# Kernel tuning notes

Hardware: AMD Instinct MI355X
Metric: run time of the kernel (lower is better)

## Reference

```python
import jax, jax.numpy as jnp
import numpy as np
import math

E = 512      # embed_dim
H = 8        # num_heads
D = E // H   # head_embed_dim
B = 1
S = 4096

def setup_inputs() -> dict:
    key = jax.random.key(0)
    ks = jax.random.split(key, 9)
    s = 1.0 / math.sqrt(E)
    return {
        "Q": jax.random.normal(ks[0], (B, S, E), dtype=jnp.float32),
        "K": jax.random.normal(ks[1], (B, S, E), dtype=jnp.float32),
        "V": jax.random.normal(ks[2], (B, S, E), dtype=jnp.float32),
        "W_qk": jax.random.uniform(ks[3], (E, E), jnp.float32, -s, s),
        "b_qk": jax.random.uniform(ks[4], (E,), jnp.float32, -s, s),
        "W_v": jax.random.uniform(ks[5], (E, E), jnp.float32, -s, s),
        "b_v": jax.random.uniform(ks[6], (E,), jnp.float32, -s, s),
        "W_out": jax.random.uniform(ks[7], (E, E), jnp.float32, -s, s),
        "b_out": jax.random.uniform(ks[8], (E,), jnp.float32, -s, s),
    }

def reference(Q, K, V, W_qk, b_qk, W_v, b_v, W_out, b_out):
    # shared qk projection (torch Linear: x @ W.T + b)
    q = Q @ W_qk.T + b_qk
    k = K @ W_qk.T + b_qk
    v = V @ W_v.T + b_v
    # NOTE: original uses .view(B, H, S, D) -- a pure reshape, no transpose
    q = q.reshape(B, H, S, D)
    k = k.reshape(B, H, S, D)
    v = v.reshape(B, H, S, D)
    scores = jnp.einsum("bhsd,bhtd->bhst", q, k) / math.sqrt(D)
    attn = jax.nn.softmax(scores, axis=-1)
    out = jnp.einsum("bhst,bhtd->bhsd", attn, v)
    out = out.reshape(B, S, E)  # matches .view merge
    return out @ W_out.T + b_out
```

## Files before the change

kernel.cpp:

```cpp
#include <hip/hip_runtime.h>
#include <hip/hip_bf16.h>
#include <math.h>

typedef __hip_bfloat16 hbf16;
typedef __attribute__((ext_vector_type(4))) float f32x4;
typedef __attribute__((ext_vector_type(8))) __bf16 bf16x8;

#define MFMA16(a, b, c) __builtin_amdgcn_mfma_f32_16x16x32_bf16((a), (b), (c), 0, 0, 0)

__device__ __forceinline__ void gload_lds16(const hbf16* g, hbf16* l) {
  __builtin_amdgcn_global_load_lds(
      (const __attribute__((address_space(1))) void*)g,
      (__attribute__((address_space(3))) void*)l, 16, 0, 0);
}

__device__ __forceinline__ void cvt4(const float* __restrict__ s, hbf16* __restrict__ d, int i) {
  float4 v = reinterpret_cast<const float4*>(s)[i];
  union { hbf16 h[4]; uint2 u; } pk;
  pk.h[0] = __float2bfloat16(v.x);
  pk.h[1] = __float2bfloat16(v.y);
  pk.h[2] = __float2bfloat16(v.z);
  pk.h[3] = __float2bfloat16(v.w);
  reinterpret_cast<uint2*>(d)[i] = pk.u;
}

__global__ __launch_bounds__(256) void cvt3_kernel(
    const float* __restrict__ s0, const float* __restrict__ s1, const float* __restrict__ s2,
    hbf16* __restrict__ d0, hbf16* __restrict__ d1, hbf16* __restrict__ d2, int n4) {
  int stride = gridDim.x * blockDim.x;
  for (int i = blockIdx.x * blockDim.x + threadIdx.x; i < n4; i += stride) {
    cvt4(s0, d0, i);
    cvt4(s1, d1, i);
    cvt4(s2, d2, i);
  }
}

__device__ __forceinline__ void gemm_core_128(
    const hbf16* __restrict__ A, const hbf16* __restrict__ B, int K, int bm, int bn,
    hbf16* Alds, hbf16* Blds, f32x4 (&acc)[4][4]) {
  const int tid = threadIdx.x;
  const int lane = tid & 63;
  const int wave = tid >> 6;
  const int wr = wave >> 1, wc = wave & 1;
  const int l15 = lane & 15, lg = lane >> 4;
  const hbf16* Abase = A + (size_t)bm * 128 * K;
  const hbf16* Bbase = B + (size_t)bn * 128 * K;
  for (int k0 = 0; k0 < K; k0 += 32) {
    if (k0) __syncthreads();
#pragma unroll
    for (int rr = 0; rr < 2; ++rr) {
      int chunk = rr * 256 + tid;
      int row = chunk >> 2;
      int c8 = (chunk & 3) << 3;
      gload_lds16(Abase + (size_t)row * K + k0 + c8, Alds + (rr * 4 + wave) * 512);
      gload_lds16(Bbase + (size_t)row * K + k0 + c8, Blds + (rr * 4 + wave) * 512);
    }
    __syncthreads();
    bf16x8 af[4], bfv[4];
#pragma unroll
    for (int m = 0; m < 4; ++m)
      af[m] = *reinterpret_cast<const bf16x8*>(&Alds[(wr * 64 + m * 16 + l15) * 32 + lg * 8]);
#pragma unroll
    for (int n = 0; n < 4; ++n)
      bfv[n] = *reinterpret_cast<const bf16x8*>(&Blds[(wc * 64 + n * 16 + l15) * 32 + lg * 8]);
#pragma unroll
    for (int m = 0; m < 4; ++m)
#pragma unroll
      for (int n = 0; n < 4; ++n)
        acc[m][n] = MFMA16(af[m], bfv[n], acc[m][n]);
  }
}

__global__ __launch_bounds__(256) void proj_qk_kernel(
    const hbf16* __restrict__ Qb, const hbf16* __restrict__ Kb,
    const hbf16* __restrict__ Wqk, const float* __restrict__ bqk,
    hbf16* __restrict__ qp, hbf16* __restrict__ kp) {
  __shared__ __align__(16) hbf16 Alds[128 * 32];
  __shared__ __align__(16) hbf16 Blds[128 * 32];
  const int z = blockIdx.y;
  const hbf16* A = z ? Kb : Qb;
  hbf16* outp = z ? kp : qp;
  const int bm = blockIdx.x & 31, bn = blockIdx.x >> 5;

  f32x4 acc[4][4];
  const f32x4 zero = {0.f, 0.f, 0.f, 0.f};
#pragma unroll
  for (int m = 0; m < 4; ++m)
#pragma unroll
    for (int n = 0; n < 4; ++n) acc[m][n] = zero;

  gemm_core_128(A, Wqk, 512, bm, bn, Alds, Blds, acc);

  const float qscale = z ? 1.0f : 0.125f * 1.4426950408889634f;

  const int lane = threadIdx.x & 63, wave = threadIdx.x >> 6;
  const int wr = wave >> 1, wc = wave & 1;
  const int l15 = lane & 15, lg = lane >> 4;
  const int row0 = bm * 128 + wr * 64;
  const int col0 = bn * 128 + wc * 64;
#pragma unroll
  for (int m = 0; m < 4; ++m) {
#pragma unroll
    for (int n = 0; n < 4; ++n) {
      const int col = col0 + n * 16 + l15;
      const float bsv = bqk[col];
#pragma unroll
      for (int j = 0; j < 4; ++j) {
        const int row = row0 + m * 16 + lg * 4 + j;
        outp[(size_t)row * 512 + col] = __float2bfloat16((acc[m][n][j] + bsv) * qscale);
      }
    }
  }
}

__global__ __launch_bounds__(256) void proj_v_kernel(
    const hbf16* __restrict__ Wv, const hbf16* __restrict__ Vb,
    const float* __restrict__ bv, hbf16* __restrict__ vT) {
  __shared__ __align__(16) hbf16 Alds[128 * 32];
  __shared__ __align__(16) hbf16 Blds[128 * 32];
  const int bm = blockIdx.x >> 5;
  const int bn = blockIdx.x & 31;

  f32x4 acc[4][4];
  const f32x4 zero = {0.f, 0.f, 0.f, 0.f};
#pragma unroll
  for (int m = 0; m < 4; ++m)
#pragma unroll
    for (int n = 0; n < 4; ++n) acc[m][n] = zero;

  gemm_core_128(Wv, Vb, 512, bm, bn, Alds, Blds, acc);

  const int lane = threadIdx.x & 63, wave = threadIdx.x >> 6;
  const int wr = wave >> 1, wc = wave & 1;
  const int l15 = lane & 15, lg = lane >> 4;
  const int row0 = bm * 128 + wr * 64;
  const int col0 = bn * 128 + wc * 64;
#pragma unroll
  for (int m = 0; m < 4; ++m) {
#pragma unroll
    for (int n = 0; n < 4; ++n) {
      const int col = col0 + n * 16 + l15;
#pragma unroll
      for (int j = 0; j < 4; ++j) {
        const int row = row0 + m * 16 + lg * 4 + j;
        const int h = col >> 9;
        const int p = ((col & 511) << 3) + (row >> 6);
        const int d = row & 63;
        vT[(size_t)h * 262144 + (size_t)d * 4096 + p] =
            __float2bfloat16(acc[m][n][j] + bv[row]);
      }
    }
  }
}

__global__ __launch_bounds__(256) void out_gemm_kernel(
    const hbf16* __restrict__ A, const hbf16* __restrict__ B, const float* __restrict__ bias,
    float* __restrict__ out) {
  __shared__ __align__(16) hbf16 Alds[128 * 32];
  __shared__ __align__(16) hbf16 Blds[128 * 32];
  const int bm = blockIdx.x & 31, bn = blockIdx.x >> 5;
  f32x4 acc[4][4];
  const f32x4 zero = {0.f, 0.f, 0.f, 0.f};
#pragma unroll
  for (int m = 0; m < 4; ++m)
#pragma unroll
    for (int n = 0; n < 4; ++n) acc[m][n] = zero;

  gemm_core_128(A, B, 512, bm, bn, Alds, Blds, acc);

  const int lane = threadIdx.x & 63, wave = threadIdx.x >> 6;
  const int wr = wave >> 1, wc = wave & 1;
  const int l15 = lane & 15, lg = lane >> 4;
  const int row0 = bm * 128 + wr * 64;
  const int col0 = bn * 128 + wc * 64;
#pragma unroll
  for (int m = 0; m < 4; ++m) {
#pragma unroll
    for (int n = 0; n < 4; ++n) {
      const int col = col0 + n * 16 + l15;
      const float bsv = bias[col];
#pragma unroll
      for (int j = 0; j < 4; ++j) {
        const int row = row0 + m * 16 + lg * 4 + j;
        out[(size_t)row * 512 + col] = acc[m][n][j] + bsv;
      }
    }
  }
}

__device__ __forceinline__ void stage64(const hbf16* __restrict__ g, int gstride,
                                        hbf16* tile, int wave, int lane) {
#pragma unroll
  for (int ii = 0; ii < 2; ++ii) {
    const int i = wave * 2 + ii;
    const int row = i * 8 + (lane >> 3);
    const int ce = ((lane & 7) ^ (lane >> 3)) << 3;
    gload_lds16(g + (size_t)row * gstride + ce, tile + i * 512);
  }
}

template <bool DIRECT>
__global__ __launch_bounds__(256) void attn_kernel2(
    const hbf16* __restrict__ qp, const hbf16* __restrict__ kp,
    const hbf16* __restrict__ vT, hbf16* __restrict__ ao,
    float* __restrict__ Opart, float* __restrict__ Lpart,
    int kv_per_split, int nwg) {
  const int lin = blockIdx.x + 32 * (blockIdx.y + 8 * blockIdx.z);
  const int chunk = nwg >> 3;
  const int swz = (lin & 7) * chunk + (lin >> 3);
  const int qt = swz & 31;
  const int h = (swz >> 5) & 7;
  const int split = swz >> 8;

  const hbf16* qh = qp + (size_t)h * 262144;
  const hbf16* kh = kp + (size_t)h * 262144;
  const hbf16* vh = vT + (size_t)h * 262144;

  const int lane = threadIdx.x & 63, wave = threadIdx.x >> 6;
  const int l15 = lane & 15, lg = lane >> 4;
  const int qrow0 = qt * 128 + wave * 32;
  const int kv0 = split * kv_per_split;
  const int nkt = kv_per_split >> 6;

  __shared__ __align__(16) hbf16 Kt[2][4096];
  __shared__ __align__(16) hbf16 Vt[2][4096];
  __shared__ __align__(16) hbf16 Pl[4][2][16][68];

  bf16x8 qf[2][2];
#pragma unroll
  for (int rb = 0; rb < 2; ++rb)
#pragma unroll
    for (int dc = 0; dc < 2; ++dc)
      qf[rb][dc] = *reinterpret_cast<const bf16x8*>(
          &qh[(size_t)(qrow0 + rb * 16 + l15) * 64 + dc * 32 + lg * 8]);

  float lsum[2][4];
  f32x4 oacc[2][4];
  const f32x4 zero = {0.f, 0.f, 0.f, 0.f};
#pragma unroll
  for (int rb = 0; rb < 2; ++rb)
#pragma unroll
    for (int j = 0; j < 4; ++j) lsum[rb][j] = 0.f;
#pragma unroll
  for (int rb = 0; rb < 2; ++rb)
#pragma unroll
    for (int db = 0; db < 4; ++db) oacc[rb][db] = zero;

  stage64(kh + (size_t)kv0 * 64, 64, Kt[0], wave, lane);
  stage64(vh + kv0, 4096, Vt[0], wave, lane);
  __syncthreads();

  int cur = 0;
  for (int t = 0; t < nkt; ++t) {
    if (t + 1 < nkt) {
      const int kb = kv0 + (t + 1) * 64;
      stage64(kh + (size_t)kb * 64, 64, Kt[cur ^ 1], wave, lane);
      stage64(vh + kb, 4096, Vt[cur ^ 1], wave, lane);
    }
    const hbf16* Kc = Kt[cur];
    const hbf16* Vc = Vt[cur];

    f32x4 s[2][4];
#pragma unroll
    for (int rb = 0; rb < 2; ++rb)
#pragma unroll
      for (int cb = 0; cb < 4; ++cb) s[rb][cb] = zero;
#pragma unroll
    for (int cb = 0; cb < 4; ++cb) {
      const int krow = cb * 16 + l15;
      const int sw = l15 & 7;
#pragma unroll
      for (int dc = 0; dc < 2; ++dc) {
        bf16x8 kf = *reinterpret_cast<const bf16x8*>(
            &Kc[krow * 64 + (((dc * 4 + lg) ^ sw) << 3)]);
#pragma unroll
        for (int rb = 0; rb < 2; ++rb) s[rb][cb] = MFMA16(qf[rb][dc], kf, s[rb][cb]);
      }
    }

#pragma unroll
    for (int rb = 0; rb < 2; ++rb)
#pragma unroll
      for (int cb = 0; cb < 4; ++cb)
#pragma unroll
        for (int j = 0; j < 4; ++j) {
          const float p = exp2f(s[rb][cb][j]);
          lsum[rb][j] += p;
          Pl[wave][rb][lg * 4 + j][cb * 16 + l15] = __float2bfloat16(p);
        }
    bf16x8 pa[2][2];
#pragma unroll
    for (int rb = 0; rb < 2; ++rb)
#pragma unroll
      for (int kc = 0; kc < 2; ++kc)
        pa[rb][kc] = *reinterpret_cast<const bf16x8*>(&Pl[wave][rb][l15][kc * 32 + lg * 8]);

#pragma unroll
    for (int db = 0; db < 4; ++db) {
      const int vrow = db * 16 + l15;
      const int sw = l15 & 7;
#pragma unroll
      for (int kc = 0; kc < 2; ++kc) {
        bf16x8 vf = *reinterpret_cast<const bf16x8*>(
            &Vc[vrow * 64 + (((kc * 4 + lg) ^ sw) << 3)]);
#pragma unroll
        for (int rb = 0; rb < 2; ++rb) oacc[rb][db] = MFMA16(pa[rb][kc], vf, oacc[rb][db]);
      }
    }
    __syncthreads();
    cur ^= 1;
  }

#pragma unroll
  for (int rb = 0; rb < 2; ++rb)
#pragma unroll
    for (int j = 0; j < 4; ++j) {
#pragma unroll
      for (int d = 1; d < 16; d <<= 1) lsum[rb][j] += __shfl_xor(lsum[rb][j], d);
    }
  if (DIRECT) {
    hbf16* oh = ao + (size_t)h * 262144;
#pragma unroll
    for (int rb = 0; rb < 2; ++rb)
#pragma unroll
      for (int j = 0; j < 4; ++j) {
        const float inv = 1.f / lsum[rb][j];
        const int row = qrow0 + rb * 16 + lg * 4 + j;
#pragma unroll
        for (int db = 0; db < 4; ++db)
          oh[(size_t)row * 64 + db * 16 + l15] = __float2bfloat16(oacc[rb][db][j] * inv);
      }
  } else {
    const size_t hrow0 = (size_t)split * 32768 + (size_t)h * 4096;
#pragma unroll
    for (int rb = 0; rb < 2; ++rb)
#pragma unroll
      for (int j = 0; j < 4; ++j) {
        const int row = qrow0 + rb * 16 + lg * 4 + j;
#pragma unroll
        for (int db = 0; db < 4; ++db)
          Opart[(hrow0 + row) * 64 + db * 16 + l15] = oacc[rb][db][j];
        if (l15 == 0) Lpart[hrow0 + row] = lsum[rb][j];
      }
  }
}

__global__ __launch_bounds__(256) void attn_combine_kernel(
    const float* __restrict__ Opart, const float* __restrict__ Lpart,
    hbf16* __restrict__ ao, int splits) {
  const int t = threadIdx.x;
  const int hrow = blockIdx.x * 64 + (t >> 2);
  const int d0 = (t & 3) * 16;
  float denom = 0.f;
  for (int s = 0; s < splits; ++s) denom += Lpart[s * 32768 + hrow];
  const float inv = 1.f / denom;
  float4 acc[4] = {};
  for (int s = 0; s < splits; ++s) {
    const float4* p = reinterpret_cast<const float4*>(
        Opart + ((size_t)s * 32768 + hrow) * 64 + d0);
#pragma unroll
    for (int i = 0; i < 4; ++i) {
      float4 v = p[i];
      acc[i].x += v.x; acc[i].y += v.y; acc[i].z += v.z; acc[i].w += v.w;
    }
  }
  union { hbf16 h[16]; uint4 u[2]; } pk;
#pragma unroll
  for (int i = 0; i < 4; ++i) {
    pk.h[i * 4 + 0] = __float2bfloat16(acc[i].x * inv);
    pk.h[i * 4 + 1] = __float2bfloat16(acc[i].y * inv);
    pk.h[i * 4 + 2] = __float2bfloat16(acc[i].z * inv);
    pk.h[i * 4 + 3] = __float2bfloat16(acc[i].w * inv);
  }
  uint4* dst = reinterpret_cast<uint4*>(ao + (size_t)hrow * 64 + d0);
  dst[0] = pk.u[0];
  dst[1] = pk.u[1];
}

extern "C" void kernel_launch(void* const* d_in, const int* in_sizes, int n_in,
                              void* d_out, int out_size, void* d_ws, size_t ws_size,
                              hipStream_t stream) {
  const float* Q = (const float*)d_in[0];
  const float* K = (const float*)d_in[1];
  const float* V = (const float*)d_in[2];
  const float* Wqk = (const float*)d_in[3];
  const float* bqk = (const float*)d_in[4];
  const float* Wv = (const float*)d_in[5];
  const float* bv = (const float*)d_in[6];
  const float* Wout = (const float*)d_in[7];
  const float* bout = (const float*)d_in[8];
  float* out = (float*)d_out;

  const size_t NE = (size_t)4096 * 512;
  const size_t WE = (size_t)512 * 512;
  hbf16* ws = (hbf16*)d_ws;
  hbf16* Qb = ws;
  hbf16* Kb = Qb + NE;
  hbf16* Vb = Kb + NE;
  hbf16* Wqkb = Vb + NE;
  hbf16* Wvb = Wqkb + WE;
  hbf16* Woutb = Wvb + WE;
  hbf16* qp = Woutb + WE;
  hbf16* kp = qp + NE;
  hbf16* vT = kp + NE;
  hbf16* ao = vT + NE;

  const size_t base_bytes = (((size_t)(7 * NE + 3 * WE) * 2) + 255) & ~(size_t)255;
  const size_t per_split_bytes = ((size_t)32768 * 64 + 32768) * 4;
  int splits = 1;
  if (ws_size >= base_bytes + 4 * per_split_bytes) splits = 4;
  else if (ws_size >= base_bytes + 2 * per_split_bytes) splits = 2;
  float* Opart = (float*)((char*)d_ws + base_bytes);
  float* Lpart = Opart + (size_t)splits * 32768 * 64;

  cvt3_kernel<<<2048, 256, 0, stream>>>(Q, K, V, Qb, Kb, Vb, (int)(NE / 4));
  cvt3_kernel<<<256, 256, 0, stream>>>(Wqk, Wv, Wout, Wqkb, Wvb, Woutb, (int)(WE / 4));
  proj_qk_kernel<<<dim3(128, 2), 256, 0, stream>>>(Qb, Kb, Wqkb, bqk, qp, kp);
  proj_v_kernel<<<128, 256, 0, stream>>>(Wvb, Vb, bv, vT);
  if (splits == 1) {
    attn_kernel2<true><<<dim3(32, 8, 1), 256, 0, stream>>>(
        qp, kp, vT, ao, nullptr, nullptr, 4096, 256);
  } else {
    attn_kernel2<false><<<dim3(32, 8, splits), 256, 0, stream>>>(
        qp, kp, vT, nullptr, Opart, Lpart, 4096 / splits, 256 * splits);
    attn_combine_kernel<<<512, 256, 0, stream>>>(Opart, Lpart, ao, splits);
  }
  out_gemm_kernel<<<128, 256, 0, stream>>>(ao, Woutb, bout, out);
}
```

Baseline: 209.9 us.

## Fuse conversion and projection launches; keep P in registers via transposed scores

The two fp32-to-bf16 conversion launches are merged into one kernel, and the QK and V projection kernels are merged into a single three-slice grid, which removes launch overhead and lets the projections run concurrently. In the attention kernel the score MFMA operands are swapped so S comes out transposed. P is then repacked into bf16 A-fragments with cross-lane shuffles instead of a round trip through LDS, which drops the per-wave P buffer and its barrier traffic. The row sums now reduce over lane groups, launch bounds request 4 blocks per CU, and the extra shuffles add VALU work.

```diff
diff --git a/kernel.cpp b/kernel.cpp
--- a/kernel.cpp
+++ b/kernel.cpp
@@ -24,14 +24,22 @@
   reinterpret_cast<uint2*>(d)[i] = pk.u;
 }
 
-__global__ __launch_bounds__(256) void cvt3_kernel(
-    const float* __restrict__ s0, const float* __restrict__ s1, const float* __restrict__ s2,
-    hbf16* __restrict__ d0, hbf16* __restrict__ d1, hbf16* __restrict__ d2, int n4) {
+__global__ __launch_bounds__(256) void cvt_all_kernel(
+    const float* __restrict__ Q, const float* __restrict__ K, const float* __restrict__ V,
+    const float* __restrict__ Wqk, const float* __restrict__ Wv, const float* __restrict__ Wout,
+    hbf16* __restrict__ Qb, hbf16* __restrict__ Kb, hbf16* __restrict__ Vb,
+    hbf16* __restrict__ Wqkb, hbf16* __restrict__ Wvb, hbf16* __restrict__ Woutb,
+    int n4big, int n4w) {
   int stride = gridDim.x * blockDim.x;
-  for (int i = blockIdx.x * blockDim.x + threadIdx.x; i < n4; i += stride) {
-    cvt4(s0, d0, i);
-    cvt4(s1, d1, i);
-    cvt4(s2, d2, i);
+  for (int i = blockIdx.x * blockDim.x + threadIdx.x; i < n4big; i += stride) {
+    cvt4(Q, Qb, i);
+    cvt4(K, Kb, i);
+    cvt4(V, Vb, i);
+    if (i < n4w) {
+      cvt4(Wqk, Wqkb, i);
+      cvt4(Wv, Wvb, i);
+      cvt4(Wout, Woutb, i);
+    }
   }
 }
 
@@ -71,55 +79,17 @@
   }
 }
 
-__global__ __launch_bounds__(256) void proj_qk_kernel(
-    const hbf16* __restrict__ Qb, const hbf16* __restrict__ Kb,
-    const hbf16* __restrict__ Wqk, const float* __restrict__ bqk,
-    hbf16* __restrict__ qp, hbf16* __restrict__ kp) {
+__global__ __launch_bounds__(256) void proj_fused_kernel(
+    const hbf16* __restrict__ Qb, const hbf16* __restrict__ Kb, const hbf16* __restrict__ Vb,
+    const hbf16* __restrict__ Wqk, const hbf16* __restrict__ Wv,
+    const float* __restrict__ bqk, const float* __restrict__ bv,
+    hbf16* __restrict__ qp, hbf16* __restrict__ kp, hbf16* __restrict__ vT) {
   __shared__ __align__(16) hbf16 Alds[128 * 32];
   __shared__ __align__(16) hbf16 Blds[128 * 32];
   const int z = blockIdx.y;
-  const hbf16* A = z ? Kb : Qb;
-  hbf16* outp = z ? kp : qp;
-  const int bm = blockIdx.x & 31, bn = blockIdx.x >> 5;
-
-  f32x4 acc[4][4];
-  const f32x4 zero = {0.f, 0.f, 0.f, 0.f};
-#pragma unroll
-  for (int m = 0; m < 4; ++m)
-#pragma unroll
-    for (int n = 0; n < 4; ++n) acc[m][n] = zero;
-
-  gemm_core_128(A, Wqk, 512, bm, bn, Alds, Blds, acc);
-
-  const float qscale = z ? 1.0f : 0.125f * 1.4426950408889634f;
-
   const int lane = threadIdx.x & 63, wave = threadIdx.x >> 6;
   const int wr = wave >> 1, wc = wave & 1;
   const int l15 = lane & 15, lg = lane >> 4;
-  const int row0 = bm * 128 + wr * 64;
-  const int col0 = bn * 128 + wc * 64;
-#pragma unroll
-  for (int m = 0; m < 4; ++m) {
-#pragma unroll
-    for (int n = 0; n < 4; ++n) {
-      const int col = col0 + n * 16 + l15;
-      const float bsv = bqk[col];
-#pragma unroll
-      for (int j = 0; j < 4; ++j) {
-        const int row = row0 + m * 16 + lg * 4 + j;
-        outp[(size_t)row * 512 + col] = __float2bfloat16((acc[m][n][j] + bsv) * qscale);
-      }
-    }
-  }
-}
-
-__global__ __launch_bounds__(256) void proj_v_kernel(
-    const hbf16* __restrict__ Wv, const hbf16* __restrict__ Vb,
-    const float* __restrict__ bv, hbf16* __restrict__ vT) {
-  __shared__ __align__(16) hbf16 Alds[128 * 32];
-  __shared__ __align__(16) hbf16 Blds[128 * 32];
-  const int bm = blockIdx.x >> 5;
-  const int bn = blockIdx.x & 31;
 
   f32x4 acc[4][4];
   const f32x4 zero = {0.f, 0.f, 0.f, 0.f};
@@ -128,26 +98,47 @@
 #pragma unroll
     for (int n = 0; n < 4; ++n) acc[m][n] = zero;
 
-  gemm_core_128(Wv, Vb, 512, bm, bn, Alds, Blds, acc);
-
-  const int lane = threadIdx.x & 63, wave = threadIdx.x >> 6;
-  const int wr = wave >> 1, wc = wave & 1;
-  const int l15 = lane & 15, lg = lane >> 4;
-  const int row0 = bm * 128 + wr * 64;
-  const int col0 = bn * 128 + wc * 64;
-#pragma unroll
-  for (int m = 0; m < 4; ++m) {
-#pragma unroll
-    for (int n = 0; n < 4; ++n) {
-      const int col = col0 + n * 16 + l15;
-#pragma unroll
-      for (int j = 0; j < 4; ++j) {
-        const int row = row0 + m * 16 + lg * 4 + j;
-        const int h = col >> 9;
-        const int p = ((col & 511) << 3) + (row >> 6);
-        const int d = row & 63;
-        vT[(size_t)h * 262144 + (size_t)d * 4096 + p] =
-            __float2bfloat16(acc[m][n][j] + bv[row]);
+  if (z < 2) {
+    const hbf16* A = z ? Kb : Qb;
+    hbf16* outp = z ? kp : qp;
+    const int bm = blockIdx.x & 31, bn = blockIdx.x >> 5;
+    gemm_core_128(A, Wqk, 512, bm, bn, Alds, Blds, acc);
+    const float qscale = z ? 1.0f : 0.125f * 1.4426950408889634f;
+    const int row0 = bm * 128 + wr * 64;
+    const int col0 = bn * 128 + wc * 64;
+#pragma unroll
+    for (int m = 0; m < 4; ++m) {
+#pragma unroll
+      for (int n = 0; n < 4; ++n) {
+        const int col = col0 + n * 16 + l15;
+        const float bsv = bqk[col];
+#pragma unroll
+        for (int j = 0; j < 4; ++j) {
+          const int row = row0 + m * 16 + lg * 4 + j;
+          outp[(size_t)row * 512 + col] = __float2bfloat16((acc[m][n][j] + bsv) * qscale);
+        }
+      }
+    }
+  } else {
+    const int bm = blockIdx.x >> 5;
+    const int bn = blockIdx.x & 31;
+    gemm_core_128(Wv, Vb, 512, bm, bn, Alds, Blds, acc);
+    const int row0 = bm * 128 + wr * 64;
+    const int col0 = bn * 128 + wc * 64;
+#pragma unroll
+    for (int m = 0; m < 4; ++m) {
+#pragma unroll
+      for (int n = 0; n < 4; ++n) {
+        const int col = col0 + n * 16 + l15;
+#pragma unroll
+        for (int j = 0; j < 4; ++j) {
+          const int row = row0 + m * 16 + lg * 4 + j;
+          const int h = col >> 9;
+          const int p = ((col & 511) << 3) + (row >> 6);
+          const int d = row & 63;
+          vT[(size_t)h * 262144 + (size_t)d * 4096 + p] =
+              __float2bfloat16(acc[m][n][j] + bv[row]);
+        }
       }
     }
   }
@@ -200,7 +191,7 @@
 }
 
 template <bool DIRECT>
-__global__ __launch_bounds__(256) void attn_kernel2(
+__global__ __launch_bounds__(256, 4) void attn_kernel3(
     const hbf16* __restrict__ qp, const hbf16* __restrict__ kp,
     const hbf16* __restrict__ vT, hbf16* __restrict__ ao,
     float* __restrict__ Opart, float* __restrict__ Lpart,
@@ -224,7 +215,6 @@
 
   __shared__ __align__(16) hbf16 Kt[2][4096];
   __shared__ __align__(16) hbf16 Vt[2][4096];
-  __shared__ __align__(16) hbf16 Pl[4][2][16][68];
 
   bf16x8 qf[2][2];
 #pragma unroll
@@ -234,13 +224,9 @@
       qf[rb][dc] = *reinterpret_cast<const bf16x8*>(
           &qh[(size_t)(qrow0 + rb * 16 + l15) * 64 + dc * 32 + lg * 8]);
 
-  float lsum[2][4];
+  float lsum[2] = {0.f, 0.f};
   f32x4 oacc[2][4];
   const f32x4 zero = {0.f, 0.f, 0.f, 0.f};
-#pragma unroll
-  for (int rb = 0; rb < 2; ++rb)
-#pragma unroll
-    for (int j = 0; j < 4; ++j) lsum[rb][j] = 0.f;
 #pragma unroll
   for (int rb = 0; rb < 2; ++rb)
 #pragma unroll
@@ -265,40 +251,55 @@
     for (int rb = 0; rb < 2; ++rb)
 #pragma unroll
       for (int cb = 0; cb < 4; ++cb) s[rb][cb] = zero;
+    const int sw = l15 & 7;
 #pragma unroll
     for (int cb = 0; cb < 4; ++cb) {
       const int krow = cb * 16 + l15;
-      const int sw = l15 & 7;
 #pragma unroll
       for (int dc = 0; dc < 2; ++dc) {
         bf16x8 kf = *reinterpret_cast<const bf16x8*>(
             &Kc[krow * 64 + (((dc * 4 + lg) ^ sw) << 3)]);
 #pragma unroll
-        for (int rb = 0; rb < 2; ++rb) s[rb][cb] = MFMA16(qf[rb][dc], kf, s[rb][cb]);
-      }
-    }
-
-#pragma unroll
-    for (int rb = 0; rb < 2; ++rb)
-#pragma unroll
-      for (int cb = 0; cb < 4; ++cb)
-#pragma unroll
-        for (int j = 0; j < 4; ++j) {
-          const float p = exp2f(s[rb][cb][j]);
-          lsum[rb][j] += p;
-          Pl[wave][rb][lg * 4 + j][cb * 16 + l15] = __float2bfloat16(p);
+        for (int rb = 0; rb < 2; ++rb) s[rb][cb] = MFMA16(kf, qf[rb][dc], s[rb][cb]);
+      }
+    }
+
+    bf16x8 pa[2][2];
+#pragma unroll
+    for (int rb = 0; rb < 2; ++rb) {
+      unsigned pr[4][2];
+#pragma unroll
+      for (int cb = 0; cb < 4; ++cb) {
+#pragma unroll
+        for (int jp = 0; jp < 2; ++jp) {
+          const float p0 = exp2f(s[rb][cb][jp * 2]);
+          const float p1 = exp2f(s[rb][cb][jp * 2 + 1]);
+          lsum[rb] += p0 + p1;
+          union { hbf16 h[2]; unsigned u; } pk;
+          pk.h[0] = __float2bfloat16(p0);
+          pk.h[1] = __float2bfloat16(p1);
+          pr[cb][jp] = pk.u;
         }
-    bf16x8 pa[2][2];
-#pragma unroll
-    for (int rb = 0; rb < 2; ++rb)
-#pragma unroll
-      for (int kc = 0; kc < 2; ++kc)
-        pa[rb][kc] = *reinterpret_cast<const bf16x8*>(&Pl[wave][rb][l15][kc * 32 + lg * 8]);
+      }
+      union { unsigned w[4]; bf16x8 v; } fr0, fr1;
+#pragma unroll
+      for (int w = 0; w < 4; ++w) {
+        const int src = l15 + ((lg & 1) << 5) + ((w >> 1) << 4);
+        const unsigned a0 = (unsigned)__shfl((int)pr[0][w & 1], src);
+        const unsigned a1 = (unsigned)__shfl((int)pr[1][w & 1], src);
+        const unsigned a2 = (unsigned)__shfl((int)pr[2][w & 1], src);
+        const unsigned a3 = (unsigned)__shfl((int)pr[3][w & 1], src);
+        const bool hi = lg >= 2;
+        fr0.w[w] = hi ? a1 : a0;
+        fr1.w[w] = hi ? a3 : a2;
+      }
+      pa[rb][0] = fr0.v;
+      pa[rb][1] = fr1.v;
+    }
 
 #pragma unroll
     for (int db = 0; db < 4; ++db) {
       const int vrow = db * 16 + l15;
-      const int sw = l15 & 7;
 #pragma unroll
       for (int kc = 0; kc < 2; ++kc) {
         bf16x8 vf = *reinterpret_cast<const bf16x8*>(
@@ -312,36 +313,36 @@
   }
 
 #pragma unroll
-  for (int rb = 0; rb < 2; ++rb)
-#pragma unroll
-    for (int j = 0; j < 4; ++j) {
-#pragma unroll
-      for (int d = 1; d < 16; d <<= 1) lsum[rb][j] += __shfl_xor(lsum[rb][j], d);
-    }
+  for (int rb = 0; rb < 2; ++rb) {
+    lsum[rb] += __shfl_xor(lsum[rb], 16);
+    lsum[rb] += __shfl_xor(lsum[rb], 32);
+  }
   if (DIRECT) {
     hbf16* oh = ao + (size_t)h * 262144;
 #pragma unroll
-    for (int rb = 0; rb < 2; ++rb)
+    for (int rb = 0; rb < 2; ++rb) {
 #pragma unroll
       for (int j = 0; j < 4; ++j) {
-        const float inv = 1.f / lsum[rb][j];
+        const float inv = 1.f / __shfl(lsum[rb], (lane & 48) | (lg * 4 + j));
         const int row = qrow0 + rb * 16 + lg * 4 + j;
 #pragma unroll
         for (int db = 0; db < 4; ++db)
           oh[(size_t)row * 64 + db * 16 + l15] = __float2bfloat16(oacc[rb][db][j] * inv);
       }
+    }
   } else {
     const size_t hrow0 = (size_t)split * 32768 + (size_t)h * 4096;
 #pragma unroll
-    for (int rb = 0; rb < 2; ++rb)
+    for (int rb = 0; rb < 2; ++rb) {
 #pragma unroll
       for (int j = 0; j < 4; ++j) {
         const int row = qrow0 + rb * 16 + lg * 4 + j;
 #pragma unroll
         for (int db = 0; db < 4; ++db)
           Opart[(hrow0 + row) * 64 + db * 16 + l15] = oacc[rb][db][j];
-        if (l15 == 0) Lpart[hrow0 + row] = lsum[rb][j];
-      }
+      }
+      if (lane < 16) Lpart[hrow0 + qrow0 + rb * 16 + lane] = lsum[rb];
+    }
   }
 }
 
@@ -413,15 +414,16 @@
   float* Opart = (float*)((char*)d_ws + base_bytes);
   float* Lpart = Opart + (size_t)splits * 32768 * 64;
 
-  cvt3_kernel<<<2048, 256, 0, stream>>>(Q, K, V, Qb, Kb, Vb, (int)(NE / 4));
-  cvt3_kernel<<<256, 256, 0, stream>>>(Wqk, Wv, Wout, Wqkb, Wvb, Woutb, (int)(WE / 4));
-  proj_qk_kernel<<<dim3(128, 2), 256, 0, stream>>>(Qb, Kb, Wqkb, bqk, qp, kp);
-  proj_v_kernel<<<128, 256, 0, stream>>>(Wvb, Vb, bv, vT);
+  cvt_all_kernel<<<2048, 256, 0, stream>>>(Q, K, V, Wqk, Wv, Wout,
+                                           Qb, Kb, Vb, Wqkb, Wvb, Woutb,
+                                           (int)(NE / 4), (int)(WE / 4));
+  proj_fused_kernel<<<dim3(128, 3), 256, 0, stream>>>(Qb, Kb, Vb, Wqkb, Wvb, bqk, bv,
+                                                      qp, kp, vT);
   if (splits == 1) {
-    attn_kernel2<true><<<dim3(32, 8, 1), 256, 0, stream>>>(
+    attn_kernel3<true><<<dim3(32, 8, 1), 256, 0, stream>>>(
         qp, kp, vT, ao, nullptr, nullptr, 4096, 256);
   } else {
-    attn_kernel2<false><<<dim3(32, 8, splits), 256, 0, stream>>>(
+    attn_kernel3<false><<<dim3(32, 8, splits), 256, 0, stream>>>(
         qp, kp, vT, nullptr, Opart, Lpart, 4096 / splits, 256 * splits);
     attn_combine_kernel<<<512, 256, 0, stream>>>(Opart, Lpart, ao, splits);
   }
```

Measured after the change: 186.6 us. 11.1% less time.
